# Optimization experiments

Hardware: AMD Instinct MI355X
Metric: run time of the kernel (lower is better)

Reference implementation:

```python
import jax, jax.numpy as jnp
import numpy as np

DIM = 2048
N_HEADS = 16
Q_LORA = 1536
KV_LORA = 512
NOPE = 128
ROPE = 64
V_DIM = 128
QK_HEAD = NOPE + ROPE
SEQ = 4096
THETA = 10000.0
EPS = 1e-6
SCALE = QK_HEAD ** -0.5  # max_seq_len==4096 not >4096, so no mscale adjustment


def rms_norm(x, w):
    return x * jax.lax.rsqrt(jnp.mean(x * x, axis=-1, keepdims=True) + EPS) * w


def rope_cos_sin(seqlen):
    inv_freq = 1.0 / THETA ** (jnp.arange(0, ROPE, 2, dtype=jnp.float32) / ROPE)  # [ROPE/2]
    t = jnp.arange(seqlen, dtype=jnp.float32)
    freqs = jnp.outer(t, inv_freq)  # [S, ROPE/2]
    return jnp.cos(freqs), jnp.sin(freqs)


def apply_rope(x, cos, sin):
    # x: (b, s, h, ROPE); pairs (x0, x1) rotated as complex mult, interleaved layout
    b, s, h, d = x.shape
    xr = x.reshape(b, s, h, d // 2, 2)
    x0, x1 = xr[..., 0], xr[..., 1]
    c = cos[None, :, None, :]
    sn = sin[None, :, None, :]
    out = jnp.stack([x0 * c - x1 * sn, x0 * sn + x1 * c], axis=-1)
    return out.reshape(b, s, h, d)


def setup_inputs() -> dict:
    key = jax.random.key(0)
    ks = jax.random.split(key, 8)
    s = lambda fan_in: 1.0 / np.sqrt(fan_in)
    return {
        "x": jax.random.normal(ks[0], (1, SEQ, DIM), jnp.float32),
        "wq_a_w": jax.random.normal(ks[1], (Q_LORA, DIM), jnp.float32) * s(DIM),
        "q_norm_w": 1.0 + 0.02 * jax.random.normal(ks[2], (Q_LORA,), jnp.float32),
        "wq_b_w": jax.random.normal(ks[3], (N_HEADS * QK_HEAD, Q_LORA), jnp.float32) * s(Q_LORA),
        "wkv_a_w": jax.random.normal(ks[4], (KV_LORA + ROPE, DIM), jnp.float32) * s(DIM),
        "kv_norm_w": 1.0 + 0.02 * jax.random.normal(ks[5], (KV_LORA,), jnp.float32),
        "wkv_b_w": jax.random.normal(ks[6], (N_HEADS * (NOPE + V_DIM), KV_LORA), jnp.float32) * s(KV_LORA),
        "wo_w": jax.random.normal(ks[7], (DIM, DIM), jnp.float32) * s(DIM),
    }


def reference(x, wq_a_w, q_norm_w, wq_b_w, wkv_a_w, kv_norm_w, wkv_b_w, wo_w):
    b, seqlen, _ = x.shape
    cos, sin = rope_cos_sin(seqlen)

    # Q path: low-rank down-proj -> RMSNorm -> up-proj
    q = rms_norm(x @ wq_a_w.T, q_norm_w) @ wq_b_w.T
    q = q.reshape(b, seqlen, N_HEADS, QK_HEAD)
    q_nope, q_pe = q[..., :NOPE], q[..., NOPE:]
    q_pe = apply_rope(q_pe, cos, sin)

    # KV path: compressed latent + decoupled rope key
    kv_a = x @ wkv_a_w.T  # (b, s, KV_LORA + ROPE)
    kv_latent, k_pe_raw = kv_a[..., :KV_LORA], kv_a[..., KV_LORA:]
    kv = rms_norm(kv_latent, kv_norm_w)               # (b, t, c)
    k_pe = apply_rope(k_pe_raw[:, :, None, :], cos, sin)[:, :, 0, :]  # (b, t, r)

    # Absorption trick: fold wkv_b's K-part into q_nope, attend against latents
    wkv_b = wkv_b_w.reshape(N_HEADS, NOPE + V_DIM, KV_LORA)
    q_abs = jnp.einsum("bshd,hdc->bshc", q_nope, wkv_b[:, :NOPE])

    scores = (jnp.einsum("bshc,btc->bsht", q_abs, kv)
              + jnp.einsum("bshr,btr->bsht", q_pe, k_pe)) * SCALE

    # causal additive mask over (s_query, t_key)
    causal = jnp.tril(jnp.ones((seqlen, seqlen), dtype=bool))
    scores = jnp.where(causal[None, :, None, :], scores, jnp.float32(-1e30))
    attn = jax.nn.softmax(scores, axis=-1)

    # post-softmax: aggregate latents, then recover V via wkv_b's V-part
    ctx = jnp.einsum("bsht,btc->bshc", attn, kv)
    v = jnp.einsum("bshc,hdc->bshd", ctx, wkv_b[:, NOPE:])  # (b, s, h, V_DIM)
    out = v.reshape(b, seqlen, N_HEADS * V_DIM) @ wo_w.T
    return out
```

## Files before the change

### kernel.cpp

```cpp
#include <hip/hip_runtime.h>

typedef unsigned short u16;
typedef __attribute__((ext_vector_type(8))) short bf16x8;
typedef __attribute__((ext_vector_type(4))) float f32x4;
typedef __attribute__((ext_vector_type(4))) unsigned short u16x4;

#define MFMA16(a, b, c) __builtin_amdgcn_mfma_f32_16x16x32_bf16((a), (b), (c), 0, 0, 0)

#define SEQ 4096
#define SCALE 0.07216878364870323f
#define LOGTHETA 9.210340371976184f

__device__ __forceinline__ u16 f2bf(float f) {
  union { float f; unsigned u; } c; c.f = f;
  unsigned u = c.u;
  unsigned r = (u + 0x7fffu + ((u >> 16) & 1u)) >> 16;
  return (u16)r;
}
__device__ __forceinline__ float bf2f(u16 b) {
  union { unsigned u; float f; } c; c.u = ((unsigned)b) << 16;
  return c.f;
}

__global__ void cvt_bf16(const float* __restrict__ src, u16* __restrict__ dst, int n4) {
  int stride = gridDim.x * blockDim.x;
  for (int i = blockIdx.x * blockDim.x + threadIdx.x; i < n4; i += stride) {
    f32x4 v = ((const f32x4*)src)[i];
    u16x4 o;
    o[0] = f2bf(v[0]); o[1] = f2bf(v[1]); o[2] = f2bf(v[2]); o[3] = f2bf(v[3]);
    ((u16x4*)dst)[i] = o;
  }
}

__global__ void trans_wkvb(const u16* __restrict__ w, u16* __restrict__ wt) {
  int stride = gridDim.x * blockDim.x;
  for (int i = blockIdx.x * blockDim.x + threadIdx.x; i < 16 * 512 * 128; i += stride) {
    int h = i >> 16;
    int r = i & 65535;
    int c = r >> 7, d = r & 127;
    wt[i] = w[(h * 256 + d) * 512 + c];
  }
}

__global__ void trans_vt(const u16* __restrict__ kva, u16* __restrict__ vt2) {
  __shared__ u16 tile[64][65];
  int c0 = blockIdx.x * 64;
  int t0 = blockIdx.y * 64;
  for (int k = 0; k < 16; k++) {
    int el = threadIdx.x + k * 256;
    int r = el >> 6, c = el & 63;
    tile[r][c] = kva[(t0 + r) * 576 + c0 + c];
  }
  __syncthreads();
  for (int k = 0; k < 16; k++) {
    int el = threadIdx.x + k * 256;
    int r = el >> 6, c = el & 63;
    int t = t0 + c;
    vt2[(t >> 5) * 16384 + (c0 + r) * 32 + (t & 31)] = tile[c][r];
  }
}

__global__ void rms_q_kernel(u16* __restrict__ qa, const float* __restrict__ w) {
  int row = blockIdx.x;
  u16* p = qa + row * 1536;
  float vals[6];
  float ss = 0.f;
#pragma unroll
  for (int k = 0; k < 6; k++) {
    float v = bf2f(p[threadIdx.x + k * 256]);
    vals[k] = v;
    ss += v * v;
  }
  for (int m = 1; m < 64; m <<= 1) ss += __shfl_xor(ss, m);
  __shared__ float red[4];
  int wid = threadIdx.x >> 6;
  if ((threadIdx.x & 63) == 0) red[wid] = ss;
  __syncthreads();
  float tot = red[0] + red[1] + red[2] + red[3];
  float rr = rsqrtf(tot / 1536.f + 1e-6f);
#pragma unroll
  for (int k = 0; k < 6; k++) {
    int i = threadIdx.x + k * 256;
    p[i] = f2bf(vals[k] * rr * w[i]);
  }
}

__global__ void rms_kv_kernel(u16* __restrict__ kva, const float* __restrict__ w) {
  int t = blockIdx.x;
  u16* p = kva + t * 576;
  float v0 = bf2f(p[threadIdx.x]);
  float v1 = bf2f(p[threadIdx.x + 256]);
  float ss = v0 * v0 + v1 * v1;
  for (int m = 1; m < 64; m <<= 1) ss += __shfl_xor(ss, m);
  __shared__ float red[4];
  int wid = threadIdx.x >> 6;
  if ((threadIdx.x & 63) == 0) red[wid] = ss;
  __syncthreads();
  float tot = red[0] + red[1] + red[2] + red[3];
  float rr = rsqrtf(tot / 512.f + 1e-6f);
  p[threadIdx.x] = f2bf(v0 * rr * w[threadIdx.x]);
  p[threadIdx.x + 256] = f2bf(v1 * rr * w[threadIdx.x + 256]);
  if (threadIdx.x < 32) {
    int i = threadIdx.x;
    float x0 = bf2f(p[512 + 2 * i]);
    float x1 = bf2f(p[512 + 2 * i + 1]);
    float invf = expf(-((float)(2 * i) / 64.f) * LOGTHETA);
    float ang = (float)t * invf;
    float cs = cosf(ang), sn = sinf(ang);
    p[512 + 2 * i] = f2bf(x0 * cs - x1 * sn);
    p[512 + 2 * i + 1] = f2bf(x0 * sn + x1 * cs);
  }
}

__global__ void rope_q_kernel(const u16* __restrict__ qb, u16* __restrict__ qcat) {
  int stride = gridDim.x * blockDim.x;
  for (int idx = blockIdx.x * blockDim.x + threadIdx.x; idx < 4096 * 512; idx += stride) {
    int s = idx >> 9;
    int r = idx & 511;
    int h = r >> 5, i = r & 31;
    float x0 = bf2f(qb[s * 3072 + h * 192 + 128 + 2 * i]);
    float x1 = bf2f(qb[s * 3072 + h * 192 + 128 + 2 * i + 1]);
    float invf = expf(-((float)(2 * i) / 64.f) * LOGTHETA);
    float ang = (float)s * invf;
    float cs = cosf(ang) * SCALE, sn = sinf(ang) * SCALE;
    qcat[s * 9216 + h * 576 + 512 + 2 * i] = f2bf(x0 * cs - x1 * sn);
    qcat[s * 9216 + h * 576 + 512 + 2 * i + 1] = f2bf(x0 * sn + x1 * cs);
  }
}

template <int BN, bool OUTF32>
__launch_bounds__(256)
__global__ void gemm_tiled(const u16* __restrict__ A, int lda, int az,
                           const u16* __restrict__ W, int ldw, int wz,
                           void* __restrict__ Cp, int ldc, int cz, int K, float oscale) {
  constexpr int NCH = 8 + BN / 16;
  constexpr int NBF = BN / 32;
  __shared__ __align__(16) u16 lds[2][NCH * 512];

  int z = blockIdx.z;
  int wid = threadIdx.x >> 6, lane = threadIdx.x & 63;
  int quad = lane >> 4, l16 = lane & 15;
  int wr = wid >> 1, wc = wid & 1;
  int m0 = blockIdx.y * 128;
  int n0 = blockIdx.x * BN;

  const u16* Az = A + (size_t)z * az;
  const u16* Wz = W + (size_t)z * wz;

  f32x4 acc[4][NBF];
#pragma unroll
  for (int i = 0; i < 4; i++)
#pragma unroll
    for (int j = 0; j < NBF; j++) acc[i][j] = {0.f, 0.f, 0.f, 0.f};

#pragma unroll
  for (int jj = 0; jj < NCH / 4; jj++) {
    int c = jj * 4 + wid;
    const u16* src = (c < 8) ? (Az + (m0 + c * 16 + l16) * (size_t)lda + quad * 8)
                             : (Wz + (n0 + (c - 8) * 16 + l16) * (size_t)ldw + quad * 8);
    __builtin_amdgcn_global_load_lds(
        (const __attribute__((address_space(1))) unsigned int*)src,
        (__attribute__((address_space(3))) unsigned int*)&lds[0][c * 512], 16, 0, 0);
  }

  int buf = 0;
  for (int k0 = 0; k0 < K; k0 += 32) {
    __syncthreads();
    if (k0 + 32 < K) {
      int k1 = k0 + 32;
#pragma unroll
      for (int jj = 0; jj < NCH / 4; jj++) {
        int c = jj * 4 + wid;
        const u16* src = (c < 8) ? (Az + (m0 + c * 16 + l16) * (size_t)lda + k1 + quad * 8)
                                 : (Wz + (n0 + (c - 8) * 16 + l16) * (size_t)ldw + k1 + quad * 8);
        __builtin_amdgcn_global_load_lds(
            (const __attribute__((address_space(1))) unsigned int*)src,
            (__attribute__((address_space(3))) unsigned int*)&lds[buf ^ 1][c * 512], 16, 0, 0);
      }
    }
    const u16* base = &lds[buf][0];
    bf16x8 a[4], b[NBF];
#pragma unroll
    for (int i = 0; i < 4; i++)
      a[i] = *(const bf16x8*)(base + (wr * 4 + i) * 512 + lane * 8);
#pragma unroll
    for (int j = 0; j < NBF; j++)
      b[j] = *(const bf16x8*)(base + (8 + wc * NBF + j) * 512 + lane * 8);
#pragma unroll
    for (int i = 0; i < 4; i++)
#pragma unroll
      for (int j = 0; j < NBF; j++) acc[i][j] = MFMA16(a[i], b[j], acc[i][j]);
    buf ^= 1;
  }

#pragma unroll
  for (int i = 0; i < 4; i++) {
    int row = m0 + wr * 64 + i * 16 + quad * 4;
#pragma unroll
    for (int j = 0; j < NBF; j++) {
      int col = n0 + wc * (BN / 2) + j * 16 + l16;
#pragma unroll
      for (int r = 0; r < 4; r++) {
        size_t cbase = (size_t)z * cz + (size_t)(row + r) * ldc + col;
        if (OUTF32) ((float*)Cp)[cbase] = acc[i][j][r] * oscale;
        else        ((u16*)Cp)[cbase] = f2bf(acc[i][j][r] * oscale);
      }
    }
  }
}

__launch_bounds__(512, 2)
__global__ void attn_kernel(const u16* __restrict__ qcat, const u16* __restrict__ kcat,
                            const u16* __restrict__ vt2, u16* __restrict__ ctx) {
  __shared__ __align__(16) u16 lds[2][34816];
  __shared__ __align__(16) u16 plds[8][16][40];

  int wid = threadIdx.x >> 6, lane = threadIdx.x & 63;
  int quad = lane >> 4, l16 = lane & 15;
  int bx = blockIdx.x;
  int h = bx & 15;
  int jb = 31 - (bx >> 4);
  int qb0 = jb << 7;
  int m0 = qb0 + wid * 16;

  bf16x8 q[18];
  {
    const u16* qb = qcat + (m0 + l16) * 9216 + h * 576 + quad * 8;
#pragma unroll
    for (int kk = 0; kk < 18; kk++) q[kk] = *(const bf16x8*)(qb + kk * 32);
  }

  f32x4 zero = {0.f, 0.f, 0.f, 0.f};
  f32x4 o[32];
#pragma unroll
  for (int ct = 0; ct < 32; ct++) o[ct] = zero;
  float li[4] = {0.f, 0.f, 0.f, 0.f};

  int nt = (qb0 >> 5) + 4;

  const u16* sp[9];
  int sstr[9], soff[9];
  bool sact[9];
#pragma unroll
  for (int jj = 0; jj < 9; jj++) {
    int c = jj * 8 + wid;
    sact[jj] = (c < 68);
    soff[jj] = c * 512;
    if (c < 36) {
      int kk = c >> 1, half = c & 1;
      sp[jj] = kcat + (half * 16 + l16) * 576 + kk * 32 + quad * 8;
      sstr[jj] = 32 * 576;
    } else {
      int ct = c - 36;
      sp[jj] = vt2 + (ct * 16 + l16) * 32 + quad * 8;
      sstr[jj] = 16384;
    }
  }

#pragma unroll
  for (int jj = 0; jj < 9; jj++) {
    if (sact[jj]) {
      __builtin_amdgcn_global_load_lds(
          (const __attribute__((address_space(1))) unsigned int*)sp[jj],
          (__attribute__((address_space(3))) unsigned int*)&lds[0][soff[jj]], 16, 0, 0);
      sp[jj] += sstr[jj];
    }
  }

  for (int ti = 0; ti < nt; ti++) {
    __syncthreads();
    int buf = ti & 1;
    if (ti + 1 < nt) {
      u16* dbase = &lds[buf ^ 1][0];
#pragma unroll
      for (int jj = 0; jj < 9; jj++) {
        if (sact[jj]) {
          __builtin_amdgcn_global_load_lds(
              (const __attribute__((address_space(1))) unsigned int*)sp[jj],
              (__attribute__((address_space(3))) unsigned int*)&dbase[soff[jj]], 16, 0, 0);
          sp[jj] += sstr[jj];
        }
      }
    }

    int t0 = ti << 5;
    if (t0 <= m0 + 15) {
      const u16* kb = &lds[buf][0];
      const u16* vb = &lds[buf][18432];
      f32x4 s0 = zero, s1 = zero;
#pragma unroll
      for (int kk = 0; kk < 18; kk++) {
        bf16x8 b0 = *(const bf16x8*)(&kb[(kk * 2 + 0) * 512 + lane * 8]);
        bf16x8 b1 = *(const bf16x8*)(&kb[(kk * 2 + 1) * 512 + lane * 8]);
        s0 = MFMA16(q[kk], b0, s0);
        s1 = MFMA16(q[kk], b1, s1);
      }
      int tc0 = t0 + l16, tc1 = t0 + 16 + l16;
#pragma unroll
      for (int r = 0; r < 4; r++) {
        int mrow = m0 + quad * 4 + r;
        float e0 = (tc0 <= mrow) ? __expf(s0[r]) : 0.f;
        float e1 = (tc1 <= mrow) ? __expf(s1[r]) : 0.f;
        li[r] += e0 + e1;
        plds[wid][quad * 4 + r][l16] = f2bf(e0);
        plds[wid][quad * 4 + r][16 + l16] = f2bf(e1);
      }
      __threadfence_block();
      bf16x8 ap = *(const bf16x8*)(&plds[wid][l16][quad * 8]);
#pragma unroll
      for (int ct = 0; ct < 32; ct++) {
        bf16x8 bv = *(const bf16x8*)(&vb[ct * 512 + lane * 8]);
        o[ct] = MFMA16(ap, bv, o[ct]);
      }
    }
  }

#pragma unroll
  for (int r = 0; r < 4; r++) {
    float s = li[r];
    s += __shfl_xor(s, 1);
    s += __shfl_xor(s, 2);
    s += __shfl_xor(s, 4);
    s += __shfl_xor(s, 8);
    li[r] = s;
  }
  f32x4 inv = {1.f / li[0], 1.f / li[1], 1.f / li[2], 1.f / li[3]};
#pragma unroll
  for (int ct = 0; ct < 32; ct++) {
    f32x4 val = o[ct] * inv;
    int base = (m0 + quad * 4) * 8192 + h * 512 + ct * 16 + l16;
    ctx[base] = f2bf(val[0]);
    ctx[base + 8192] = f2bf(val[1]);
    ctx[base + 2 * 8192] = f2bf(val[2]);
    ctx[base + 3 * 8192] = f2bf(val[3]);
  }
}

extern "C" void kernel_launch(void* const* d_in, const int* in_sizes, int n_in,
                              void* d_out, int out_size, void* d_ws, size_t ws_size,
                              hipStream_t stream) {
  const float* x = (const float*)d_in[0];
  const float* wqa = (const float*)d_in[1];
  const float* qnw = (const float*)d_in[2];
  const float* wqb = (const float*)d_in[3];
  const float* wkva = (const float*)d_in[4];
  const float* kvnw = (const float*)d_in[5];
  const float* wkvb = (const float*)d_in[6];
  const float* wo = (const float*)d_in[7];

  u16* ws = (u16*)d_ws;
  u16* XB = ws;
  u16* WQAB = ws + 8388608;
  u16* WQBB = ws + 11534336;
  u16* WKVAB = ws + 16252928;
  u16* WKVBB = ws + 17432576;
  u16* WKVBT = ws + 19529728;
  u16* WOB = ws + 20578304;
  u16* QA = ws + 24772608;
  u16* KVA = ws + 31064064;
  u16* VT = ws + 33423360;
  u16* QCAT = ws + 35520512;
  u16* CTX = ws + 73269248;
  u16* QB = CTX;
  u16* VBUF = QCAT;

  dim3 blk(256);

  cvt_bf16<<<1024, blk, 0, stream>>>(x, XB, 2097152);
  cvt_bf16<<<1024, blk, 0, stream>>>(wqa, WQAB, 786432);
  cvt_bf16<<<1024, blk, 0, stream>>>(wqb, WQBB, 1179648);
  cvt_bf16<<<1024, blk, 0, stream>>>(wkva, WKVAB, 294912);
  cvt_bf16<<<1024, blk, 0, stream>>>(wkvb, WKVBB, 524288);
  cvt_bf16<<<1024, blk, 0, stream>>>(wo, WOB, 1048576);
  trans_wkvb<<<1024, blk, 0, stream>>>(WKVBB, WKVBT);

  gemm_tiled<128, false><<<dim3(12, 32, 1), blk, 0, stream>>>(XB, 2048, 0, WQAB, 2048, 0, QA, 1536, 0, 2048, 1.f);
  gemm_tiled<64, false><<<dim3(9, 32, 1), blk, 0, stream>>>(XB, 2048, 0, WKVAB, 2048, 0, KVA, 576, 0, 2048, 1.f);

  rms_q_kernel<<<4096, blk, 0, stream>>>(QA, qnw);
  rms_kv_kernel<<<4096, blk, 0, stream>>>(KVA, kvnw);
  trans_vt<<<dim3(8, 64), blk, 0, stream>>>(KVA, VT);

  gemm_tiled<128, false><<<dim3(24, 32, 1), blk, 0, stream>>>(QA, 1536, 0, WQBB, 1536, 0, QB, 3072, 0, 1536, 1.f);

  gemm_tiled<128, false><<<dim3(4, 32, 16), blk, 0, stream>>>(QB, 3072, 192, WKVBT, 128, 65536, QCAT, 9216, 576, 128, SCALE);
  rope_q_kernel<<<2048, blk, 0, stream>>>(QB, QCAT);

  attn_kernel<<<512, dim3(512), 0, stream>>>(QCAT, KVA, VT, CTX);

  gemm_tiled<128, false><<<dim3(1, 32, 16), blk, 0, stream>>>(CTX, 8192, 512, WKVBB + 65536, 512, 131072, VBUF, 2048, 128, 512, 1.f);

  gemm_tiled<128, true><<<dim3(16, 32, 1), blk, 0, stream>>>(VBUF, 2048, 0, WOB, 2048, 0, d_out, 2048, 0, 2048, 1.f);
}
```

Measured before the change: 928.2 us.

## Repartition PV accumulation across waves as 4 row-groups by column-groups with barrier

Instead of each wave computing the full 16x512 output tile for its own 16 query rows, waves now share P through LDS: each wave handles 64 rows (4 row fragments) by 128 latent columns. The goal is to read each V fragment from LDS once per four row fragments instead of once per row, cutting LDS traffic for V. The cost is an extra block-wide barrier every key tile and a normalization step at the end that goes through LDS. It also sets s_setprio around the MFMA loops.

```diff
diff --git a/kernel.cpp b/kernel.cpp
--- a/kernel.cpp
+++ b/kernel.cpp
@@ -214,6 +214,7 @@
                             const u16* __restrict__ vt2, u16* __restrict__ ctx) {
   __shared__ __align__(16) u16 lds[2][34816];
   __shared__ __align__(16) u16 plds[8][16][40];
+  __shared__ __align__(16) float linv[128];
 
   int wid = threadIdx.x >> 6, lane = threadIdx.x & 63;
   int quad = lane >> 4, l16 = lane & 15;
@@ -222,6 +223,7 @@
   int jb = 31 - (bx >> 4);
   int qb0 = jb << 7;
   int m0 = qb0 + wid * 16;
+  int rg = wid >> 2, cg = wid & 3;
 
   bf16x8 q[18];
   {
@@ -231,9 +233,12 @@
   }
 
   f32x4 zero = {0.f, 0.f, 0.f, 0.f};
-  f32x4 o[32];
-#pragma unroll
-  for (int ct = 0; ct < 32; ct++) o[ct] = zero;
+  bf16x8 apz = {0, 0, 0, 0, 0, 0, 0, 0};
+  f32x4 o[4][8];
+#pragma unroll
+  for (int rf = 0; rf < 4; rf++)
+#pragma unroll
+    for (int ct = 0; ct < 8; ct++) o[rf][ct] = zero;
   float li[4] = {0.f, 0.f, 0.f, 0.f};
 
   int nt = (qb0 >> 5) + 4;
@@ -286,8 +291,8 @@
     int t0 = ti << 5;
     if (t0 <= m0 + 15) {
       const u16* kb = &lds[buf][0];
-      const u16* vb = &lds[buf][18432];
       f32x4 s0 = zero, s1 = zero;
+      __builtin_amdgcn_s_setprio(1);
 #pragma unroll
       for (int kk = 0; kk < 18; kk++) {
         bf16x8 b0 = *(const bf16x8*)(&kb[(kk * 2 + 0) * 512 + lane * 8]);
@@ -295,6 +300,7 @@
         s0 = MFMA16(q[kk], b0, s0);
         s1 = MFMA16(q[kk], b1, s1);
       }
+      __builtin_amdgcn_s_setprio(0);
       int tc0 = t0 + l16, tc1 = t0 + 16 + l16;
 #pragma unroll
       for (int r = 0; r < 4; r++) {
@@ -305,13 +311,30 @@
         plds[wid][quad * 4 + r][l16] = f2bf(e0);
         plds[wid][quad * 4 + r][16 + l16] = f2bf(e1);
       }
-      __threadfence_block();
-      bf16x8 ap = *(const bf16x8*)(&plds[wid][l16][quad * 8]);
-#pragma unroll
-      for (int ct = 0; ct < 32; ct++) {
-        bf16x8 bv = *(const bf16x8*)(&vb[ct * 512 + lane * 8]);
-        o[ct] = MFMA16(ap, bv, o[ct]);
-      }
+    }
+
+    asm volatile("s_waitcnt lgkmcnt(0)" ::: "memory");
+    __builtin_amdgcn_s_barrier();
+    __builtin_amdgcn_sched_barrier(0);
+
+    if (t0 <= qb0 + rg * 64 + 63) {
+      const u16* vb = &lds[buf][18432];
+      __builtin_amdgcn_s_setprio(1);
+#pragma unroll
+      for (int hp = 0; hp < 2; hp++) {
+        int g0 = rg * 4 + hp * 2;
+        bf16x8 ap0 = (t0 <= qb0 + g0 * 16 + 15)
+                         ? *(const bf16x8*)(&plds[g0][l16][quad * 8]) : apz;
+        bf16x8 ap1 = (t0 <= qb0 + g0 * 16 + 31)
+                         ? *(const bf16x8*)(&plds[g0 + 1][l16][quad * 8]) : apz;
+#pragma unroll
+        for (int ct = 0; ct < 8; ct++) {
+          bf16x8 bv = *(const bf16x8*)(&vb[(cg * 8 + ct) * 512 + lane * 8]);
+          o[hp * 2 + 0][ct] = MFMA16(ap0, bv, o[hp * 2 + 0][ct]);
+          o[hp * 2 + 1][ct] = MFMA16(ap1, bv, o[hp * 2 + 1][ct]);
+        }
+      }
+      __builtin_amdgcn_s_setprio(0);
     }
   }
 
@@ -324,15 +347,24 @@
     s += __shfl_xor(s, 8);
     li[r] = s;
   }
-  f32x4 inv = {1.f / li[0], 1.f / li[1], 1.f / li[2], 1.f / li[3]};
-#pragma unroll
-  for (int ct = 0; ct < 32; ct++) {
-    f32x4 val = o[ct] * inv;
-    int base = (m0 + quad * 4) * 8192 + h * 512 + ct * 16 + l16;
-    ctx[base] = f2bf(val[0]);
-    ctx[base + 8192] = f2bf(val[1]);
-    ctx[base + 2 * 8192] = f2bf(val[2]);
-    ctx[base + 3 * 8192] = f2bf(val[3]);
+  if (l16 == 0) {
+#pragma unroll
+    for (int r = 0; r < 4; r++) linv[wid * 16 + quad * 4 + r] = 1.f / li[r];
+  }
+  __syncthreads();
+#pragma unroll
+  for (int rf = 0; rf < 4; rf++) {
+    int g = rg * 4 + rf;
+    f32x4 iv = *(const f32x4*)(&linv[g * 16 + quad * 4]);
+#pragma unroll
+    for (int ct = 0; ct < 8; ct++) {
+      f32x4 val = o[rf][ct];
+      int base = (qb0 + g * 16 + quad * 4) * 8192 + h * 512 + cg * 128 + ct * 16 + l16;
+      ctx[base] = f2bf(val[0] * iv[0]);
+      ctx[base + 8192] = f2bf(val[1] * iv[1]);
+      ctx[base + 2 * 8192] = f2bf(val[2] * iv[2]);
+      ctx[base + 3 * 8192] = f2bf(val[3] * iv[3]);
+    }
   }
 }
 
```

New measurement: 1.210 ms. 30.3% more time.
